# Kernel tuning notes

Hardware: AMD Instinct MI355X
Metric: run time of the kernel (lower is better)

The kernel has to match this reference:

```python
import jax, jax.numpy as jnp
import numpy as np
import math

IMAGE_SIZE = 512
N_ANGLES = 180
BATCH = 4


def _shepp_logan_filter(size):
    # Matches _get_fourier_filter(size, 'shepp-logan') in the torch module.
    n = np.concatenate([np.arange(1, size // 2 + 1, 2), np.arange(size // 2 - 1, 0, -2)])
    f = np.zeros(size, dtype=np.float64)
    f[0] = 0.25
    f[1::2] = -1.0 / (np.pi * n) ** 2
    ff = 2.0 * np.real(np.fft.fft(f))
    omega = np.pi * np.fft.fftfreq(size)[1:]
    ff[1:] *= np.sin(omega) / omega
    return jnp.asarray(ff, dtype=jnp.float32)


def setup_inputs() -> dict:
    key = jax.random.key(0)
    sinogram = jax.random.normal(key, (BATCH, N_ANGLES, IMAGE_SIZE), dtype=jnp.float32)
    return {"sinogram": sinogram}


def _inverse_radon(sinogram):
    B, A, P = sinogram.shape
    S = P  # image_size == proj_size (required by the torch filter expand)
    # --- FFT ramp filtering (pad_size == P for power-of-two P >= 64, so pad_width = 0) ---
    ff = _shepp_logan_filter(P)  # [P]
    filtered = jnp.real(
        jnp.fft.ifft(jnp.fft.fft(sinogram, axis=-1) * ff, axis=-1)
    ).astype(sinogram.dtype)  # [B, A, P]

    # --- backprojection grid (note: x axis is reversed, as in the torch meshgrid) ---
    x = jnp.arange(S - 1, -1, -1, dtype=jnp.float32) - S // 2  # [W]
    y = jnp.arange(S, dtype=jnp.float32) - S // 2              # [H]
    angles_rad = jnp.linspace(0.0, 180.0, A) * (math.pi / 180.0)  # [A]
    half = P // 2

    def body(acc, inp):
        theta, row = inp  # theta scalar, row: [B, P] filtered projection for this angle
        # unnormalized sample position; equals grid_sample(align_corners=True) coord
        p = x[None, :] * jnp.sin(theta) + y[:, None] * jnp.cos(theta) + half  # [H, W]
        i0f = jnp.floor(p)
        frac = p - i0f  # [H, W]
        i0 = i0f.astype(jnp.int32)
        i1 = i0 + 1

        def tap(idx):
            # bilinear tap with zeros padding (out-of-range taps contribute 0)
            valid = (idx >= 0) & (idx <= P - 1)  # [H, W]
            v = jnp.take(row, jnp.clip(idx, 0, P - 1), axis=1)  # [B, H, W]
            return jnp.where(valid[None], v, jnp.zeros((), dtype=row.dtype))

        contrib = (1.0 - frac)[None] * tap(i0) + frac[None] * tap(i1)  # [B, H, W]
        return acc + contrib, None

    out0 = jnp.zeros((B, S, S), dtype=sinogram.dtype)
    out, _ = jax.lax.scan(body, out0, (angles_rad, jnp.swapaxes(filtered, 0, 1)))
    out = out * (math.pi / (2.0 * A))

    # circle mask
    radius = S // 2
    mask = (x[None, :] ** 2 + y[:, None] ** 2) <= radius ** 2  # [H, W]
    out = out * mask[None].astype(out.dtype)
    return out[:, None]  # [B, 1, S, S]


def reference(sinogram):
    return _inverse_radon(sinogram)
```

## Files before the change

kernel.cpp:

```cpp
#include <hip/hip_runtime.h>
#include <math.h>

#define P      512
#define NA     180
#define NB     4
#define FS2    1056
#define FOFF2  16
#define GUARD  512
#define TS     16
#define WSF    56
#define ASEG   60
#define NTILES (32 * 32)

#if __has_builtin(__builtin_amdgcn_fractf)
#define FRACT(x) __builtin_amdgcn_fractf(x)
#else
#define FRACT(x) ((x) - floorf(x))
#endif

typedef float f4g __attribute__((ext_vector_type(4), aligned(16)));
typedef float f4l __attribute__((ext_vector_type(4), aligned(8)));

__global__ __launch_bounds__(64) void ir_spectrum(float* __restrict__ ffg,
                                                  float2* __restrict__ sct) {
    const int o = blockIdx.x;
    const int t = threadIdx.x;
    double s = 0.0;
    #pragma unroll
    for (int i = 0; i < 4; ++i) {
        const int m = t + 64 * i;
        const int idx = 2 * m + 1;
        const int n = (idx < 256) ? idx : (512 - idx);
        const double fv = -1.0 / ((M_PI * n) * (M_PI * n));
        const int ph = (o * idx) & 511;
        s += fv * cos((2.0 * M_PI / 512.0) * (double)ph);
    }
    #pragma unroll
    for (int off = 32; off; off >>= 1) s += __shfl_down(s, off, 64);
    if (t == 0) {
        double ff = 0.5 + 2.0 * s;
        if (o > 0) {
            const double freq = (o <= 256) ? (double)o / 512.0 : ((double)o - 512.0) / 512.0;
            const double w = M_PI * freq;
            ff *= sin(w) / w;
        }
        ffg[o] = (float)ff;
        if (o < NA) {
            const float th = (float)o * (float)(M_PI / (double)(NA - 1));
            sct[o] = make_float2(sinf(th), cosf(th));
        }
    }
}

__global__ __launch_bounds__(64) void ir_impulse(const float* __restrict__ ffg,
                                                 float* __restrict__ hr) {
    const int o = blockIdx.x;
    const int t = threadIdx.x;
    double s = 0.0;
    #pragma unroll
    for (int i = 0; i < 8; ++i) {
        const int k = t + 64 * i;
        const int ph = (o * k) & 511;
        s += (double)ffg[k] * cos((2.0 * M_PI / 512.0) * (double)ph);
    }
    #pragma unroll
    for (int off = 32; off; off >>= 1) s += __shfl_down(s, off, 64);
    if (t == 0) hr[o] = (float)(s / 512.0);
}

__global__ __launch_bounds__(256) void ir_filter(const float* __restrict__ sino,
                                                 const float* __restrict__ hr,
                                                 float* __restrict__ fil2,
                                                 const float2* __restrict__ sct,
                                                 float* __restrict__ qbt) {
    __shared__ float row2[2][2 * P];
    const int a = blockIdx.x;
    const int p = blockIdx.y;
    const int t = threadIdx.x;

    if (p == 2) {
        const float2 sc = sct[a];
        #pragma unroll
        for (int i = 0; i < 4; ++i) {
            const int tile = t + 256 * i;
            const int bx = tile & 31, by = tile >> 5;
            const float xlo = (float)(240 - 16 * bx);
            const float ylo = (float)(16 * by - 256);
            const float yhi = (float)(16 * by - 241);
            const float pmin = fmaf(sc.x, xlo, fminf(sc.y * ylo, sc.y * yhi) + 256.0f);
            const int base = ((int)floorf(pmin) - 2) & ~1;
            qbt[tile * NA + a] = (float)(256 - base);
        }
        return;
    }

    const int r = t >> 7;
    const int tt = t & 127;
    const int b = 2 * p + r;

    const float* src = sino + ((size_t)b * NA + a) * P;
    const float4 v = *(const float4*)(src + 4 * tt);
    *(float4*)&row2[r][4 * tt] = v;
    *(float4*)&row2[r][4 * tt + P] = v;
    __syncthreads();

    const int base0 = P + 4 * tt;
    float4 A = *(const float4*)&row2[r][base0];
    float a0 = 0.f, a1 = 0.f, a2 = 0.f, a3 = 0.f;
    #pragma unroll 4
    for (int J = 0; J < P; J += 4) {
        const float4 Bv = *(const float4*)&row2[r][base0 - J - 4];
        const float h0 = hr[J], h1 = hr[J + 1], h2v = hr[J + 2], h3 = hr[J + 3];
        a0 = fmaf(h0, A.x, a0); a0 = fmaf(h1, Bv.w, a0); a0 = fmaf(h2v, Bv.z, a0); a0 = fmaf(h3, Bv.y, a0);
        a1 = fmaf(h0, A.y, a1); a1 = fmaf(h1, A.x, a1); a1 = fmaf(h2v, Bv.w, a1); a1 = fmaf(h3, Bv.z, a1);
        a2 = fmaf(h0, A.z, a2); a2 = fmaf(h1, A.y, a2); a2 = fmaf(h2v, A.x, a2); a2 = fmaf(h3, Bv.w, a2);
        a3 = fmaf(h0, A.w, a3); a3 = fmaf(h1, A.z, a3); a3 = fmaf(h2v, A.y, a3); a3 = fmaf(h3, A.x, a3);
        A = Bv;
    }
    float* frow = fil2 + ((size_t)p * NA + a) * FS2;
    const int o0 = FOFF2 + 8 * tt + r;
    frow[o0]     = a0;
    frow[o0 + 2] = a1;
    frow[o0 + 4] = a2;
    frow[o0 + 6] = a3;
    if (t < FOFF2) {
        frow[t] = 0.f;
        frow[FOFF2 + 2 * P + t] = 0.f;
    }
}

__global__ __launch_bounds__(256) void ir_backproject(const float* __restrict__ fil2,
                                                      const float2* __restrict__ sct,
                                                      const float* __restrict__ qbt,
                                                      float* __restrict__ out) {
    __shared__ float win[ASEG * WSF];

    const int t = threadIdx.x;
    const int w0 = blockIdx.x * TS, h0 = blockIdx.y * TS;
    const int p = blockIdx.z;
    const float* qrow = qbt + (blockIdx.y * 32 + blockIdx.x) * NA;

    const int w = w0 + (t & 15);
    const int h = h0 + (t >> 4);

    const int ix = 255 - w;
    const int iy = h - 256;
    const int m = (ix * ix + iy * iy) <= 256 * 256;

    float* o0 = out + (((size_t)(2 * p) * P) + h) * P + w;
    float* o1 = o0 + (size_t)P * P;

    if (__syncthreads_count(m) == 0) {
        o0[0] = 0.f;
        o1[0] = 0.f;
        return;
    }

    const float xf = (float)ix;
    const float yf = (float)iy;
    const float* fbase = fil2 + (size_t)p * NA * FS2;
    float acc0 = 0.f, acc1 = 0.f;

    #pragma unroll
    for (int seg = 0; seg < 3; ++seg) {
        const int A0 = seg * ASEG;

        for (int idx = t; idx < ASEG * (WSF / 4); idx += 256) {
            const int al = idx / (WSF / 4);
            const int i = idx - al * (WSF / 4);
            const int a = A0 + al;
            const int base = 256 - (int)qrow[a];
            const f4g vv = *(const f4g*)(fbase + a * FS2 + FOFF2 + 2 * base + 4 * i);
            *(f4g*)(win + al * WSF + 4 * i) = vv;
        }
        __syncthreads();

        #pragma unroll 4
        for (int al = 0; al < ASEG; ++al) {
            const float2 sc = sct[A0 + al];
            const float qb = qrow[A0 + al];
            const float q = fmaf(xf, sc.x, fmaf(yf, sc.y, qb));
            const int j = (int)q;
            const float fr = FRACT(q);
            const f4l W = *(const f4l*)(win + al * WSF + 2 * j);
            acc0 = fmaf(1.f - fr, W.x, fmaf(fr, W.z, acc0));
            acc1 = fmaf(1.f - fr, W.y, fmaf(fr, W.w, acc1));
        }
        if (seg < 2) __syncthreads();
    }

    const float scale = (float)(M_PI / (2.0 * NA));
    o0[0] = m ? acc0 * scale : 0.f;
    o1[0] = m ? acc1 * scale : 0.f;
}

extern "C" void kernel_launch(void* const* d_in, const int* in_sizes, int n_in,
                              void* d_out, int out_size, void* d_ws, size_t ws_size,
                              hipStream_t stream) {
    const float* sino = (const float*)d_in[0];
    float* out = (float*)d_out;
    float* ws = (float*)d_ws;

    float* ffg   = ws;
    float* hr    = ws + 512;
    float2* sct  = (float2*)(ws + 1024);
    float* qbt   = ws + 1536;
    float* fil2  = ws + 1536 + NTILES * NA + GUARD;

    ir_spectrum<<<P, 64, 0, stream>>>(ffg, sct);
    ir_impulse<<<P, 64, 0, stream>>>(ffg, hr);

    dim3 gridF(NA, 3);
    ir_filter<<<gridF, 256, 0, stream>>>(sino, hr, fil2, sct, qbt);

    dim3 gridB(P / TS, P / TS, NB / 2);
    ir_backproject<<<gridB, 256, 0, stream>>>(fil2, sct, qbt, out);
}
```

Measured before the change: 105.6 us.

## Interleave all four batches in filtered layout and backproject them per block

The filtered projections are now stored with all four batch elements interleaved per detector position, staged through shared memory so each row is written with coalesced float4 stores. The backprojection grid loses its batch dimension, so each thread accumulates four batches and the per-pixel coordinate, fraction and index work is shared across them with two aligned float4 LDS reads per angle. The sin/cos table is also computed inside the filter kernel instead of the spectrum kernel. In exchange the grid halves, leaving fewer blocks to fill the GPU, and each thread holds more registers.

```diff
diff --git a/kernel.cpp b/kernel.cpp
--- a/kernel.cpp
+++ b/kernel.cpp
@@ -4,11 +4,12 @@
 #define P      512
 #define NA     180
 #define NB     4
-#define FS2    1056
-#define FOFF2  16
+#define FOFF4  64
+#define FS4    (FOFF4 + 4 * P + FOFF4)
 #define GUARD  512
 #define TS     16
-#define WSF    56
+#define WPOS   28
+#define WSF4   (WPOS * 4)
 #define ASEG   60
 #define NTILES (32 * 32)
 
@@ -18,11 +19,9 @@
 #define FRACT(x) ((x) - floorf(x))
 #endif
 
-typedef float f4g __attribute__((ext_vector_type(4), aligned(16)));
-typedef float f4l __attribute__((ext_vector_type(4), aligned(8)));
-
-__global__ __launch_bounds__(64) void ir_spectrum(float* __restrict__ ffg,
-                                                  float2* __restrict__ sct) {
+typedef float f4 __attribute__((ext_vector_type(4), aligned(16)));
+
+__global__ __launch_bounds__(64) void ir_spectrum(float* __restrict__ ffg) {
     const int o = blockIdx.x;
     const int t = threadIdx.x;
     double s = 0.0;
@@ -45,10 +44,6 @@
             ff *= sin(w) / w;
         }
         ffg[o] = (float)ff;
-        if (o < NA) {
-            const float th = (float)o * (float)(M_PI / (double)(NA - 1));
-            sct[o] = make_float2(sinf(th), cosf(th));
-        }
     }
 }
 
@@ -68,48 +63,50 @@
     if (t == 0) hr[o] = (float)(s / 512.0);
 }
 
-__global__ __launch_bounds__(256) void ir_filter(const float* __restrict__ sino,
+__global__ __launch_bounds__(512) void ir_filter(const float* __restrict__ sino,
                                                  const float* __restrict__ hr,
                                                  float* __restrict__ fil2,
-                                                 const float2* __restrict__ sct,
+                                                 float2* __restrict__ sct,
                                                  float* __restrict__ qbt) {
-    __shared__ float row2[2][2 * P];
+    __shared__ __align__(16) float row2[4][2 * P];
+    __shared__ __align__(16) float sOut[4 * P];
     const int a = blockIdx.x;
-    const int p = blockIdx.y;
-    const int t = threadIdx.x;
-
-    if (p == 2) {
-        const float2 sc = sct[a];
+    const int t = threadIdx.x;
+
+    if (blockIdx.y == 1) {
+        const float th = (float)a * (float)(M_PI / (double)(NA - 1));
+        const float s = sinf(th);
+        const float c = cosf(th);
+        if (t == 0) sct[a] = make_float2(s, c);
         #pragma unroll
-        for (int i = 0; i < 4; ++i) {
-            const int tile = t + 256 * i;
+        for (int i = 0; i < 2; ++i) {
+            const int tile = t + 512 * i;
             const int bx = tile & 31, by = tile >> 5;
             const float xlo = (float)(240 - 16 * bx);
             const float ylo = (float)(16 * by - 256);
             const float yhi = (float)(16 * by - 241);
-            const float pmin = fmaf(sc.x, xlo, fminf(sc.y * ylo, sc.y * yhi) + 256.0f);
+            const float pmin = fmaf(s, xlo, fminf(c * ylo, c * yhi) + 256.0f);
             const int base = ((int)floorf(pmin) - 2) & ~1;
             qbt[tile * NA + a] = (float)(256 - base);
         }
         return;
     }
 
-    const int r = t >> 7;
+    const int b = t >> 7;
     const int tt = t & 127;
-    const int b = 2 * p + r;
 
     const float* src = sino + ((size_t)b * NA + a) * P;
     const float4 v = *(const float4*)(src + 4 * tt);
-    *(float4*)&row2[r][4 * tt] = v;
-    *(float4*)&row2[r][4 * tt + P] = v;
+    *(float4*)&row2[b][4 * tt] = v;
+    *(float4*)&row2[b][4 * tt + P] = v;
     __syncthreads();
 
     const int base0 = P + 4 * tt;
-    float4 A = *(const float4*)&row2[r][base0];
+    float4 A = *(const float4*)&row2[b][base0];
     float a0 = 0.f, a1 = 0.f, a2 = 0.f, a3 = 0.f;
     #pragma unroll 4
     for (int J = 0; J < P; J += 4) {
-        const float4 Bv = *(const float4*)&row2[r][base0 - J - 4];
+        const float4 Bv = *(const float4*)&row2[b][base0 - J - 4];
         const float h0 = hr[J], h1 = hr[J + 1], h2v = hr[J + 2], h3 = hr[J + 3];
         a0 = fmaf(h0, A.x, a0); a0 = fmaf(h1, Bv.w, a0); a0 = fmaf(h2v, Bv.z, a0); a0 = fmaf(h3, Bv.y, a0);
         a1 = fmaf(h0, A.y, a1); a1 = fmaf(h1, A.x, a1); a1 = fmaf(h2v, Bv.w, a1); a1 = fmaf(h3, Bv.z, a1);
@@ -117,15 +114,18 @@
         a3 = fmaf(h0, A.w, a3); a3 = fmaf(h1, A.z, a3); a3 = fmaf(h2v, A.y, a3); a3 = fmaf(h3, A.x, a3);
         A = Bv;
     }
-    float* frow = fil2 + ((size_t)p * NA + a) * FS2;
-    const int o0 = FOFF2 + 8 * tt + r;
-    frow[o0]     = a0;
-    frow[o0 + 2] = a1;
-    frow[o0 + 4] = a2;
-    frow[o0 + 6] = a3;
-    if (t < FOFF2) {
+    const int o0 = 16 * tt + b;
+    sOut[o0]      = a0;
+    sOut[o0 + 4]  = a1;
+    sOut[o0 + 8]  = a2;
+    sOut[o0 + 12] = a3;
+    __syncthreads();
+
+    float* frow = fil2 + (size_t)a * FS4;
+    *(f4*)(frow + FOFF4 + 4 * t) = *(const f4*)(sOut + 4 * t);
+    if (t < FOFF4) {
         frow[t] = 0.f;
-        frow[FOFF2 + 2 * P + t] = 0.f;
+        frow[FOFF4 + 4 * P + t] = 0.f;
     }
 }
 
@@ -133,11 +133,10 @@
                                                       const float2* __restrict__ sct,
                                                       const float* __restrict__ qbt,
                                                       float* __restrict__ out) {
-    __shared__ float win[ASEG * WSF];
+    __shared__ __align__(16) float win[ASEG * WSF4 + 16];
 
     const int t = threadIdx.x;
     const int w0 = blockIdx.x * TS, h0 = blockIdx.y * TS;
-    const int p = blockIdx.z;
     const float* qrow = qbt + (blockIdx.y * 32 + blockIdx.x) * NA;
 
     const int w = w0 + (t & 15);
@@ -147,31 +146,32 @@
     const int iy = h - 256;
     const int m = (ix * ix + iy * iy) <= 256 * 256;
 
-    float* o0 = out + (((size_t)(2 * p) * P) + h) * P + w;
-    float* o1 = o0 + (size_t)P * P;
+    float* o0 = out + (size_t)h * P + w;
 
     if (__syncthreads_count(m) == 0) {
         o0[0] = 0.f;
-        o1[0] = 0.f;
+        o0[P * P] = 0.f;
+        o0[2 * P * P] = 0.f;
+        o0[3 * P * P] = 0.f;
         return;
     }
 
     const float xf = (float)ix;
     const float yf = (float)iy;
-    const float* fbase = fil2 + (size_t)p * NA * FS2;
-    float acc0 = 0.f, acc1 = 0.f;
+    float acc0 = 0.f, acc1 = 0.f, acc2 = 0.f, acc3 = 0.f;
 
     #pragma unroll
     for (int seg = 0; seg < 3; ++seg) {
         const int A0 = seg * ASEG;
 
-        for (int idx = t; idx < ASEG * (WSF / 4); idx += 256) {
-            const int al = idx / (WSF / 4);
-            const int i = idx - al * (WSF / 4);
+        for (int idx = t; idx < ASEG * WPOS; idx += 256) {
+            const int al = idx / WPOS;
+            const int i = idx - al * WPOS;
             const int a = A0 + al;
             const int base = 256 - (int)qrow[a];
-            const f4g vv = *(const f4g*)(fbase + a * FS2 + FOFF2 + 2 * base + 4 * i);
-            *(f4g*)(win + al * WSF + 4 * i) = vv;
+            const int off = a * FS4 + FOFF4 + 4 * (base + i);
+            const f4 vv = *(const f4*)(fil2 + off);
+            *(f4*)(win + al * WSF4 + 4 * i) = vv;
         }
         __syncthreads();
 
@@ -182,16 +182,22 @@
             const float q = fmaf(xf, sc.x, fmaf(yf, sc.y, qb));
             const int j = (int)q;
             const float fr = FRACT(q);
-            const f4l W = *(const f4l*)(win + al * WSF + 2 * j);
-            acc0 = fmaf(1.f - fr, W.x, fmaf(fr, W.z, acc0));
-            acc1 = fmaf(1.f - fr, W.y, fmaf(fr, W.w, acc1));
+            const float omf = 1.f - fr;
+            const f4 W0 = *(const f4*)(win + al * WSF4 + 4 * j);
+            const f4 W1 = *(const f4*)(win + al * WSF4 + 4 * j + 4);
+            acc0 = fmaf(omf, W0.x, fmaf(fr, W1.x, acc0));
+            acc1 = fmaf(omf, W0.y, fmaf(fr, W1.y, acc1));
+            acc2 = fmaf(omf, W0.z, fmaf(fr, W1.z, acc2));
+            acc3 = fmaf(omf, W0.w, fmaf(fr, W1.w, acc3));
         }
         if (seg < 2) __syncthreads();
     }
 
     const float scale = (float)(M_PI / (2.0 * NA));
-    o0[0] = m ? acc0 * scale : 0.f;
-    o1[0] = m ? acc1 * scale : 0.f;
+    o0[0]         = m ? acc0 * scale : 0.f;
+    o0[P * P]     = m ? acc1 * scale : 0.f;
+    o0[2 * P * P] = m ? acc2 * scale : 0.f;
+    o0[3 * P * P] = m ? acc3 * scale : 0.f;
 }
 
 extern "C" void kernel_launch(void* const* d_in, const int* in_sizes, int n_in,
@@ -207,12 +213,12 @@
     float* qbt   = ws + 1536;
     float* fil2  = ws + 1536 + NTILES * NA + GUARD;
 
-    ir_spectrum<<<P, 64, 0, stream>>>(ffg, sct);
+    ir_spectrum<<<P, 64, 0, stream>>>(ffg);
     ir_impulse<<<P, 64, 0, stream>>>(ffg, hr);
 
-    dim3 gridF(NA, 3);
-    ir_filter<<<gridF, 256, 0, stream>>>(sino, hr, fil2, sct, qbt);
-
-    dim3 gridB(P / TS, P / TS, NB / 2);
+    dim3 gridF(NA, 2);
+    ir_filter<<<gridF, 512, 0, stream>>>(sino, hr, fil2, sct, qbt);
+
+    dim3 gridB(P / TS, P / TS, 1);
     ir_backproject<<<gridB, 256, 0, stream>>>(fil2, sct, qbt, out);
 }
```

Result: faster. 102.4 us (-3.0%).
